# Performance work log

Measured on AMD Instinct MI355X. Metric: run time of the kernel, lower is better.

The kernel has to match this reference:

```python
import jax, jax.numpy as jnp
import numpy as np
from jax import lax

EPS = 1e-5
TEM = 10.0  # self.tem at init; tem_proportion buffer is 0 so it stays 10.0


def _conv1d(x, w, padding, dilation=1, groups=1):
    # x: [B, C, S], w: [O, I//groups, K]
    return lax.conv_general_dilated(
        x, w, window_strides=(1,), padding=[(padding, padding)],
        rhs_dilation=(dilation,), dimension_numbers=('NCH', 'OIH', 'NCH'),
        feature_group_count=groups)


def _bn(y, gamma, beta):
    # training-mode BatchNorm1d: stats over (batch, length) per channel
    m = y.mean(axis=(0, 2), keepdims=True)
    v = y.var(axis=(0, 2), keepdims=True)
    return (y - m) * lax.rsqrt(v + EPS) * gamma[None, :, None] + beta[None, :, None]


def _nor_conv(x, w, g, b, k):
    return _bn(_conv1d(jax.nn.relu(x), w, padding=k // 2), g, b)


def _dil_conv(x, wd, wp, g, b, k):
    C = x.shape[1]
    y = _conv1d(jax.nn.relu(x), wd, padding=k - 1, dilation=2, groups=C)
    y = _conv1d(y, wp, padding=0)
    return _bn(y, g, b)


def _avg_pool3(x):
    s = lax.reduce_window(x, 0.0, lax.add, (1, 1, 3), (1, 1, 1),
                          [(0, 0), (0, 0), (1, 1)])
    return s / 3.0  # count_include_pad=True


def _max_pool3(x):
    return lax.reduce_window(x, -jnp.inf, lax.max, (1, 1, 3), (1, 1, 1),
                             [(0, 0), (0, 0), (1, 1)])


def _forward(x, u, arch_parameters,
             w_nor3, g_nor3, b_nor3, w_nor5, g_nor5, b_nor5,
             w_nor7, g_nor7, b_nor7,
             wd_dil3, wp_dil3, g_dil3, b_dil3,
             wd_dil5, wp_dil5, g_dil5, b_dil5,
             wd_dil7, wp_dil7, g_dil7, b_dil7):
    # ---- Gumbel straight-through gate (get_gumbel_prob) ----
    uc = jnp.clip(u, 1e-9, 1.0 - 1e-9)
    gumbels = -jnp.log(-jnp.log(uc))  # -log(Exp(1) sample)
    logits = (jax.nn.log_softmax(arch_parameters, axis=1) + gumbels) / TEM
    probs = jax.nn.softmax(logits, axis=1)          # [1, 10]
    index = jnp.argmax(probs, axis=-1)              # [1]
    one_h = jax.nn.one_hot(index, probs.shape[-1], dtype=probs.dtype)
    hardwts = one_h - lax.stop_gradient(probs) + probs  # straight-through

    # ---- forward_gdas: single edge (max_nodes=2) ----
    xc = jnp.transpose(x, (0, 2, 1))  # [B, H, S]: hidden=channels, seq=length
    branches = [
        lambda t: jnp.zeros_like(t),                         # none
        _avg_pool3,                                          # avg_pool_3
        _max_pool3,                                          # max_pool_3
        lambda t: _nor_conv(t, w_nor3, g_nor3, b_nor3, 3),   # nor_conv_3
        lambda t: _nor_conv(t, w_nor5, g_nor5, b_nor5, 5),   # nor_conv_5
        lambda t: _nor_conv(t, w_nor7, g_nor7, b_nor7, 7),   # nor_conv_7
        lambda t: _dil_conv(t, wd_dil3, wp_dil3, g_dil3, b_dil3, 3),
        lambda t: _dil_conv(t, wd_dil5, wp_dil5, g_dil5, b_dil5, 5),
        lambda t: _dil_conv(t, wd_dil7, wp_dil7, g_dil7, b_dil7, 7),
        lambda t: t,                                         # skip_connect
    ]
    idx = index[0]
    w = hardwts[0]                                  # [10]
    sel = lax.switch(idx, branches, xc)             # only argmax op is run
    w_sel = jnp.take(w, idx)
    # GDAS: w[argmax]*op(x) + sum of remaining scalar weights (broadcast add)
    out = w_sel * sel + (jnp.sum(w) - w_sel)
    out = jnp.transpose(out, (0, 2, 1))             # back to [B, S, H]
    return out + x                                  # residual


def setup_inputs() -> dict:
    key = jax.random.key(0)
    ks = jax.random.split(key, 16)
    B, S, H = 8, 512, 768
    d = {
        'x': jax.random.normal(ks[0], (B, S, H), jnp.float32),
        'u': jax.random.uniform(ks[1], (1, 10), jnp.float32),
        'arch_parameters': 0.001 * jax.random.normal(ks[2], (1, 10), jnp.float32),
    }
    i = 3
    for k in (3, 5, 7):
        d[f'w_nor{k}'] = 0.02 * jax.random.normal(ks[i], (H, H, k), jnp.float32); i += 1
        d[f'g_nor{k}'] = jnp.ones((H,), jnp.float32)
        d[f'b_nor{k}'] = jnp.zeros((H,), jnp.float32)
    for k in (3, 5, 7):
        d[f'wd_dil{k}'] = 0.1 * jax.random.normal(ks[i], (H, 1, k), jnp.float32); i += 1
        d[f'wp_dil{k}'] = 0.02 * jax.random.normal(ks[i], (H, H, 1), jnp.float32); i += 1
        d[f'g_dil{k}'] = jnp.ones((H,), jnp.float32)
        d[f'b_dil{k}'] = jnp.zeros((H,), jnp.float32)
    return d


def reference(x, u, arch_parameters,
              w_nor3, g_nor3, b_nor3, w_nor5, g_nor5, b_nor5,
              w_nor7, g_nor7, b_nor7,
              wd_dil3, wp_dil3, g_dil3, b_dil3,
              wd_dil5, wp_dil5, g_dil5, b_dil5,
              wd_dil7, wp_dil7, g_dil7, b_dil7):
    return _forward(x, u, arch_parameters,
                    w_nor3, g_nor3, b_nor3, w_nor5, g_nor5, b_nor5,
                    w_nor7, g_nor7, b_nor7,
                    wd_dil3, wp_dil3, g_dil3, b_dil3,
                    wd_dil5, wp_dil5, g_dil5, b_dil5,
                    wd_dil7, wp_dil7, g_dil7, b_dil7)
```

## Files before the change

kernel.cpp:

```cpp
#include <hip/hip_runtime.h>
#include <math.h>

#define BB 8
#define SS 512
#define HH 768
#define NTOT (BB*SS*HH)
#define EPSBN 1e-5f
#define SPAD 4
#define SROWS (SS + 2*SPAD)

typedef __attribute__((ext_vector_type(8))) short short8v;
typedef __attribute__((ext_vector_type(4))) float float4v;

struct Params {
  const float *x, *u, *ap;
  const float *w_nor3, *g_nor3, *b_nor3;
  const float *w_nor5, *g_nor5, *b_nor5;
  const float *w_nor7, *g_nor7, *b_nor7;
  const float *wd3, *wp3, *gd3, *bd3;
  const float *wd5, *wp5, *gd5, *bd5;
  const float *wd7, *wp7, *gd7, *bd7;
  float *out;
  float *hdr;
  float *y;
  short *xb;
  short *wb;
  float *psum;
  float *psq;
};

__device__ __forceinline__ short f2bf(float f) {
  union { float f; unsigned u; } v; v.f = f;
  unsigned r = v.u + 0x7FFF + ((v.u >> 16) & 1);
  return (short)(r >> 16);
}

__global__ void gate_kernel(Params p) {
  int t = threadIdx.x;
  for (int i = t; i < HH; i += 64) { p.psum[i] = 0.f; p.psq[i] = 0.f; }
  if (t != 0) return;
  float ap[10], lg[10], pr[10];
  float mx = -INFINITY;
  for (int i = 0; i < 10; i++) { ap[i] = p.ap[i]; mx = fmaxf(mx, ap[i]); }
  float se = 0.f;
  for (int i = 0; i < 10; i++) se += expf(ap[i] - mx);
  float lse = mx + logf(se);
  float lmax = -INFINITY;
  for (int i = 0; i < 10; i++) {
    float uc = fminf(fmaxf(p.u[i], 1e-9f), 1.f - 1e-9f);
    float gb = -logf(-logf(uc));
    lg[i] = ((ap[i] - lse) + gb) * 0.1f;
    lmax = fmaxf(lmax, lg[i]);
  }
  float ps = 0.f;
  for (int i = 0; i < 10; i++) { pr[i] = expf(lg[i] - lmax); ps += pr[i]; }
  int idx = 0; float best = -INFINITY;
  for (int i = 0; i < 10; i++) {
    pr[i] /= ps;
    if (pr[i] > best) { best = pr[i]; idx = i; }
  }
  float w_sel = (1.0f - pr[idx]) + pr[idx];
  p.hdr[0] = w_sel;
  p.hdr[1] = 0.0f;
  ((int*)p.hdr)[2] = idx;
}

#define XBLK 1560
#define WBLK 2016
__global__ __launch_bounds__(256) void prep_kernel(Params p) {
  int idx = ((const int*)p.hdr)[2];
  if (idx < 3 || idx > 8) return;
  int t = threadIdx.x;
  if (blockIdx.x < XBLK) {
    int u = blockIdx.x * 256 + t;
    int c0 = (u % 96) * 8;
    int row = (u / 96) % SROWS;
    int b = u / (96 * SROWS);
    int s = row - SPAD;
    short8v o8 = (short8v){0,0,0,0,0,0,0,0};
    if (s >= 0 && s < SS) {
      float v[8];
      if (idx <= 5) {
        const float* xp = p.x + ((size_t)(b * SS + s) * HH + c0);
        float4 f0 = ((const float4*)xp)[0];
        float4 f1 = ((const float4*)xp)[1];
        v[0] = fmaxf(f0.x, 0.f); v[1] = fmaxf(f0.y, 0.f);
        v[2] = fmaxf(f0.z, 0.f); v[3] = fmaxf(f0.w, 0.f);
        v[4] = fmaxf(f1.x, 0.f); v[5] = fmaxf(f1.y, 0.f);
        v[6] = fmaxf(f1.z, 0.f); v[7] = fmaxf(f1.w, 0.f);
      } else {
        int k = 3 + 2 * (idx - 6);
        const float* wd = (idx == 6) ? p.wd3 : (idx == 7) ? p.wd5 : p.wd7;
#pragma unroll
        for (int j = 0; j < 8; j++) v[j] = 0.f;
        for (int dk = 0; dk < k; dk++) {
          int ss = s + 2 * dk - (k - 1);
          if (ss < 0 || ss >= SS) continue;
          const float* xp = p.x + ((size_t)(b * SS + ss) * HH + c0);
          float4 f0 = ((const float4*)xp)[0];
          float4 f1 = ((const float4*)xp)[1];
          float ff[8] = {f0.x, f0.y, f0.z, f0.w, f1.x, f1.y, f1.z, f1.w};
#pragma unroll
          for (int j = 0; j < 8; j++)
            v[j] += fmaxf(ff[j], 0.f) * wd[(c0 + j) * k + dk];
        }
      }
#pragma unroll
      for (int j = 0; j < 8; j++) o8[j] = f2bf(v[j]);
    }
    *(short8v*)(p.xb + (size_t)(b * SROWS + row) * HH + c0) = o8;
  } else {
    int u = (blockIdx.x - XBLK) * 256 + t;
    int i0 = (u % 96) * 8;
    int o = (u / 96) % HH;
    int dk = u / (96 * HH);
    short8v o8;
    if (idx <= 5) {
      int k = 3 + 2 * (idx - 3);
      if (dk >= k) return;
      const float* W = (idx == 3) ? p.w_nor3 : (idx == 4) ? p.w_nor5 : p.w_nor7;
#pragma unroll
      for (int j = 0; j < 8; j++)
        o8[j] = f2bf(W[((size_t)o * HH + i0 + j) * k + dk]);
      *(short8v*)(p.wb + ((size_t)dk * HH + o) * HH + i0) = o8;
    } else {
      if (dk != 0) return;
      const float* W = (idx == 6) ? p.wp3 : (idx == 7) ? p.wp5 : p.wp7;
      const float* wp0 = W + (size_t)o * HH + i0;
      float4 f0 = ((const float4*)wp0)[0];
      float4 f1 = ((const float4*)wp0)[1];
      o8[0] = f2bf(f0.x); o8[1] = f2bf(f0.y); o8[2] = f2bf(f0.z); o8[3] = f2bf(f0.w);
      o8[4] = f2bf(f1.x); o8[5] = f2bf(f1.y); o8[6] = f2bf(f1.z); o8[7] = f2bf(f1.w);
      *(short8v*)(p.wb + (size_t)o * HH + i0) = o8;
    }
  }
}

#define BM 128
#define BN 64
#define BK 64

typedef const __attribute__((address_space(1))) unsigned int* gas_t;
typedef __attribute__((address_space(3))) unsigned int* las_t;
__device__ __forceinline__ void gload16(const void* g, void* l) {
  __builtin_amdgcn_global_load_lds((gas_t)g, (las_t)l, 16, 0, 0);
}

__global__ __launch_bounds__(256) void conv_gemm_kernel(Params p) {
  int idx = ((const int*)p.hdr)[2];
  if (idx < 3 || idx > 8) return;
  bool nor = (idx <= 5);
  int taps = nor ? (3 + 2 * (idx - 3)) : 1;
  int halo = nor ? (taps >> 1) : 0;

  __shared__ __attribute__((aligned(16))) short As[BM * BK];
  __shared__ __attribute__((aligned(16))) short Bs[BN * BK];

  int mt = blockIdx.x;
  int b = mt >> 2;
  int s0 = (mt & 3) * BM;
  int o0 = blockIdx.y * BN;

  int t = threadIdx.x;
  int lane = t & 63;
  int w = t >> 6;
  int l16 = lane & 15, quad = lane >> 4;
  int wm0 = (w >> 1) * 64;
  int wn0 = (w & 1) * 32;
  int lr = lane >> 3;
  int sw8 = ((lane & 7) ^ lr) * 8;

  short* Al0 = &As[(32 * w) * BK];
  short* Bl0 = &Bs[(16 * w) * BK];

  float4v acc[4][2];
#pragma unroll
  for (int mi = 0; mi < 4; mi++)
#pragma unroll
    for (int ni = 0; ni < 2; ni++) acc[mi][ni] = (float4v){0.f, 0.f, 0.f, 0.f};

  const char* Ac = (const char*)As;
  const char* Bc = (const char*)Bs;
  int aro[4], bro[2], co[2];
#pragma unroll
  for (int mi = 0; mi < 4; mi++) aro[mi] = (wm0 + mi * 16 + l16) * (BK * 2);
#pragma unroll
  for (int ni = 0; ni < 2; ni++) bro[ni] = (wn0 + ni * 16 + l16) * (BK * 2);
  int sx = (l16 & 7) << 4;
  co[0] = (quad * 16) ^ sx;
  co[1] = (64 + quad * 16) ^ sx;

  for (int dk = 0; dk < taps; dk++) {
    int shift = dk - halo;
    const short* Ag[4]; const short* Bg[2];
#pragma unroll
    for (int j = 0; j < 4; j++) {
      int tr = 32 * w + 8 * j + lr;
      Ag[j] = p.xb + (size_t)(b * SROWS + SPAD + s0 + shift + tr) * HH + sw8;
    }
#pragma unroll
    for (int j = 0; j < 2; j++) {
      int tr = 16 * w + 8 * j + lr;
      Bg[j] = p.wb + ((size_t)dk * HH + o0 + tr) * HH + sw8;
    }
    for (int k0 = 0; k0 < HH; k0 += BK) {
#pragma unroll
      for (int j = 0; j < 4; j++) gload16(Ag[j] + k0, Al0 + j * 8 * BK);
#pragma unroll
      for (int j = 0; j < 2; j++) gload16(Bg[j] + k0, Bl0 + j * 8 * BK);
      __syncthreads();

      short8v af[4][2], bf[2][2];
#pragma unroll
      for (int mi = 0; mi < 4; mi++) {
        af[mi][0] = *(const short8v*)(Ac + aro[mi] + co[0]);
        af[mi][1] = *(const short8v*)(Ac + aro[mi] + co[1]);
      }
#pragma unroll
      for (int ni = 0; ni < 2; ni++) {
        bf[ni][0] = *(const short8v*)(Bc + bro[ni] + co[0]);
        bf[ni][1] = *(const short8v*)(Bc + bro[ni] + co[1]);
      }
#pragma unroll
      for (int h = 0; h < 2; h++)
#pragma unroll
        for (int mi = 0; mi < 4; mi++)
#pragma unroll
          for (int ni = 0; ni < 2; ni++)
            acc[mi][ni] = __builtin_amdgcn_mfma_f32_16x16x32_bf16(af[mi][h], bf[ni][h], acc[mi][ni], 0, 0, 0);
      __syncthreads();
    }
  }

#pragma unroll
  for (int mi = 0; mi < 4; mi++)
#pragma unroll
    for (int ni = 0; ni < 2; ni++) {
      int col = o0 + wn0 + ni * 16 + l16;
#pragma unroll
      for (int r = 0; r < 4; r++) {
        int row = s0 + wm0 + mi * 16 + quad * 4 + r;
        p.y[((size_t)(b * SS + row)) * HH + col] = acc[mi][ni][r];
      }
    }

#pragma unroll
  for (int ni = 0; ni < 2; ni++) {
    float s = 0.f, q = 0.f;
#pragma unroll
    for (int mi = 0; mi < 4; mi++)
#pragma unroll
      for (int r = 0; r < 4; r++) { float v = acc[mi][ni][r]; s += v; q += v * v; }
    s += __shfl_xor(s, 16); s += __shfl_xor(s, 32);
    q += __shfl_xor(q, 16); q += __shfl_xor(q, 32);
    if (lane < 16) {
      int col = o0 + wn0 + ni * 16 + l16;
      atomicAdd(&p.psum[col], s);
      atomicAdd(&p.psq[col], q);
    }
  }
}

__global__ __launch_bounds__(256) void epilogue_kernel(Params p) {
  int idx = ((const int*)p.hdr)[2];
  float w_sel = p.hdr[0], w_rest = p.hdr[1];
  int t4 = blockIdx.x * 256 + threadIdx.x;
  int base = t4 * 4;
  float4 xv = *(const float4*)(p.x + base);
  float4 sel;
  if (idx >= 3 && idx <= 8) {
    const float* g = (idx == 3) ? p.g_nor3 : (idx == 4) ? p.g_nor5 : (idx == 5) ? p.g_nor7
                   : (idx == 6) ? p.gd3 : (idx == 7) ? p.gd5 : p.gd7;
    const float* be = (idx == 3) ? p.b_nor3 : (idx == 4) ? p.b_nor5 : (idx == 5) ? p.b_nor7
                    : (idx == 6) ? p.bd3 : (idx == 7) ? p.bd5 : p.bd7;
    int c = base % HH;
    float4 yv = *(const float4*)(p.y + base);
    float4 ps = *(const float4*)(p.psum + c);
    float4 pq = *(const float4*)(p.psq + c);
    float4 gv = *(const float4*)(g + c);
    float4 bv = *(const float4*)(be + c);
    const float inv = 1.f / 4096.f;
    float m0 = ps.x * inv, m1 = ps.y * inv, m2 = ps.z * inv, m3 = ps.w * inv;
    float i0 = rsqrtf(pq.x * inv - m0 * m0 + EPSBN);
    float i1 = rsqrtf(pq.y * inv - m1 * m1 + EPSBN);
    float i2 = rsqrtf(pq.z * inv - m2 * m2 + EPSBN);
    float i3 = rsqrtf(pq.w * inv - m3 * m3 + EPSBN);
    sel.x = (yv.x - m0) * i0 * gv.x + bv.x;
    sel.y = (yv.y - m1) * i1 * gv.y + bv.y;
    sel.z = (yv.z - m2) * i2 * gv.z + bv.z;
    sel.w = (yv.w - m3) * i3 * gv.w + bv.w;
  } else if (idx == 0) {
    sel = (float4){0.f, 0.f, 0.f, 0.f};
  } else if (idx == 9) {
    sel = xv;
  } else {
    int s = (base / HH) % SS;
    float4 xm, xp;
    if (idx == 1) {
      xm = (s > 0)      ? *(const float4*)(p.x + base - HH) : (float4){0.f, 0.f, 0.f, 0.f};
      xp = (s < SS - 1) ? *(const float4*)(p.x + base + HH) : (float4){0.f, 0.f, 0.f, 0.f};
      const float th = 1.f / 3.f;
      sel.x = (xm.x + xv.x + xp.x) * th;
      sel.y = (xm.y + xv.y + xp.y) * th;
      sel.z = (xm.z + xv.z + xp.z) * th;
      sel.w = (xm.w + xv.w + xp.w) * th;
    } else {
      xm = (s > 0)      ? *(const float4*)(p.x + base - HH) : (float4){-INFINITY, -INFINITY, -INFINITY, -INFINITY};
      xp = (s < SS - 1) ? *(const float4*)(p.x + base + HH) : (float4){-INFINITY, -INFINITY, -INFINITY, -INFINITY};
      sel.x = fmaxf(fmaxf(xm.x, xv.x), xp.x);
      sel.y = fmaxf(fmaxf(xm.y, xv.y), xp.y);
      sel.z = fmaxf(fmaxf(xm.z, xv.z), xp.z);
      sel.w = fmaxf(fmaxf(xm.w, xv.w), xp.w);
    }
  }
  float4 ov;
  ov.x = w_sel * sel.x + w_rest + xv.x;
  ov.y = w_sel * sel.y + w_rest + xv.y;
  ov.z = w_sel * sel.z + w_rest + xv.z;
  ov.w = w_sel * sel.w + w_rest + xv.w;
  *(float4*)(p.out + base) = ov;
}

extern "C" void kernel_launch(void* const* d_in, const int* in_sizes, int n_in,
                              void* d_out, int out_size, void* d_ws, size_t ws_size,
                              hipStream_t stream) {
  Params p;
  p.x = (const float*)d_in[0];
  p.u = (const float*)d_in[1];
  p.ap = (const float*)d_in[2];
  p.w_nor3 = (const float*)d_in[3];  p.g_nor3 = (const float*)d_in[4];  p.b_nor3 = (const float*)d_in[5];
  p.w_nor5 = (const float*)d_in[6];  p.g_nor5 = (const float*)d_in[7];  p.b_nor5 = (const float*)d_in[8];
  p.w_nor7 = (const float*)d_in[9];  p.g_nor7 = (const float*)d_in[10]; p.b_nor7 = (const float*)d_in[11];
  p.wd3 = (const float*)d_in[12]; p.wp3 = (const float*)d_in[13]; p.gd3 = (const float*)d_in[14]; p.bd3 = (const float*)d_in[15];
  p.wd5 = (const float*)d_in[16]; p.wp5 = (const float*)d_in[17]; p.gd5 = (const float*)d_in[18]; p.bd5 = (const float*)d_in[19];
  p.wd7 = (const float*)d_in[20]; p.wp7 = (const float*)d_in[21]; p.gd7 = (const float*)d_in[22]; p.bd7 = (const float*)d_in[23];
  p.out = (float*)d_out;

  char* ws = (char*)d_ws;
  size_t off = 0;
  p.hdr = (float*)(ws + off); off += 256;
  p.y   = (float*)(ws + off); off += (size_t)NTOT * 4;
  p.xb  = (short*)(ws + off); off += (size_t)BB * SROWS * HH * 2;
  p.wb  = (short*)(ws + off); off += (size_t)7 * HH * HH * 2;
  p.psum = (float*)(ws + off); off += HH * 4;
  p.psq  = (float*)(ws + off); off += HH * 4;

  hipLaunchKernelGGL(gate_kernel, dim3(1), dim3(64), 0, stream, p);
  hipLaunchKernelGGL(prep_kernel, dim3(XBLK + WBLK), dim3(256), 0, stream, p);
  hipLaunchKernelGGL(conv_gemm_kernel, dim3(SS * BB / BM, HH / BN), dim3(256), 0, stream, p);
  hipLaunchKernelGGL(epilogue_kernel, dim3(NTOT / 4 / 256), dim3(256), 0, stream, p);
}
```

Baseline: 137.0 us.

## Reuse halo-extended activation tile across conv taps and vectorize weight prep

```diff
diff --git a/kernel.cpp b/kernel.cpp
--- a/kernel.cpp
+++ b/kernel.cpp
@@ -66,7 +66,24 @@
 }
 
 #define XBLK 1560
-#define WBLK 2016
+#define WBLK 288
+
+template<int K>
+__device__ __forceinline__ void wprep(const float* __restrict__ W, short* __restrict__ wb,
+                                      int o, int i0) {
+  const float* src = W + ((size_t)o * HH + i0) * K;
+  float f[8 * K];
+#pragma unroll
+  for (int j = 0; j < 2 * K; j++) ((float4*)f)[j] = ((const float4*)src)[j];
+#pragma unroll
+  for (int dk = 0; dk < K; dk++) {
+    short8v o8;
+#pragma unroll
+    for (int j = 0; j < 8; j++) o8[j] = f2bf(f[j * K + dk]);
+    *(short8v*)(wb + ((size_t)dk * HH + o) * HH + i0) = o8;
+  }
+}
+
 __global__ __launch_bounds__(256) void prep_kernel(Params p) {
   int idx = ((const int*)p.hdr)[2];
   if (idx < 3 || idx > 8) return;
@@ -112,33 +129,18 @@
   } else {
     int u = (blockIdx.x - XBLK) * 256 + t;
     int i0 = (u % 96) * 8;
-    int o = (u / 96) % HH;
-    int dk = u / (96 * HH);
-    short8v o8;
-    if (idx <= 5) {
-      int k = 3 + 2 * (idx - 3);
-      if (dk >= k) return;
-      const float* W = (idx == 3) ? p.w_nor3 : (idx == 4) ? p.w_nor5 : p.w_nor7;
-#pragma unroll
-      for (int j = 0; j < 8; j++)
-        o8[j] = f2bf(W[((size_t)o * HH + i0 + j) * k + dk]);
-      *(short8v*)(p.wb + ((size_t)dk * HH + o) * HH + i0) = o8;
-    } else {
-      if (dk != 0) return;
-      const float* W = (idx == 6) ? p.wp3 : (idx == 7) ? p.wp5 : p.wp7;
-      const float* wp0 = W + (size_t)o * HH + i0;
-      float4 f0 = ((const float4*)wp0)[0];
-      float4 f1 = ((const float4*)wp0)[1];
-      o8[0] = f2bf(f0.x); o8[1] = f2bf(f0.y); o8[2] = f2bf(f0.z); o8[3] = f2bf(f0.w);
-      o8[4] = f2bf(f1.x); o8[5] = f2bf(f1.y); o8[6] = f2bf(f1.z); o8[7] = f2bf(f1.w);
-      *(short8v*)(p.wb + (size_t)o * HH + i0) = o8;
-    }
+    int o = u / 96;
+    if (idx == 3)      wprep<3>(p.w_nor3, p.wb, o, i0);
+    else if (idx == 4) wprep<5>(p.w_nor5, p.wb, o, i0);
+    else if (idx == 5) wprep<7>(p.w_nor7, p.wb, o, i0);
+    else wprep<1>((idx == 6) ? p.wp3 : (idx == 7) ? p.wp5 : p.wp7, p.wb, o, i0);
   }
 }
 
 #define BM 128
 #define BN 64
 #define BK 64
+#define AROWS 136
 
 typedef const __attribute__((address_space(1))) unsigned int* gas_t;
 typedef __attribute__((address_space(3))) unsigned int* las_t;
@@ -146,15 +148,15 @@
   __builtin_amdgcn_global_load_lds((gas_t)g, (las_t)l, 16, 0, 0);
 }
 
-__global__ __launch_bounds__(256) void conv_gemm_kernel(Params p) {
+__global__ __launch_bounds__(256, 3) void conv_gemm_kernel(Params p) {
   int idx = ((const int*)p.hdr)[2];
   if (idx < 3 || idx > 8) return;
   bool nor = (idx <= 5);
   int taps = nor ? (3 + 2 * (idx - 3)) : 1;
   int halo = nor ? (taps >> 1) : 0;
 
-  __shared__ __attribute__((aligned(16))) short As[BM * BK];
-  __shared__ __attribute__((aligned(16))) short Bs[BN * BK];
+  __shared__ __attribute__((aligned(16))) short As[AROWS * BK];
+  __shared__ __attribute__((aligned(16))) short Bs[4 * BN * BK];
 
   int mt = blockIdx.x;
   int b = mt >> 2;
@@ -170,8 +172,18 @@
   int lr = lane >> 3;
   int sw8 = ((lane & 7) ^ lr) * 8;
 
-  short* Al0 = &As[(32 * w) * BK];
-  short* Bl0 = &Bs[(16 * w) * BK];
+  const short* Ag[4];
+  int abrow = b * SROWS + s0 + 8 * w + lr;
+#pragma unroll
+  for (int j = 0; j < 4; j++)
+    Ag[j] = p.xb + (size_t)(abrow + 32 * j) * HH + sw8;
+  const short* Agp = p.xb + (size_t)(b * SROWS + s0 + 128 + lr) * HH + sw8;
+  const short* Bg = p.wb + (size_t)(o0 + 8 * w + lr) * HH + sw8;
+
+  short* Asl[4];
+#pragma unroll
+  for (int j = 0; j < 4; j++) Asl[j] = &As[(32 * j + 8 * w) * BK];
+  short* Aslp = &As[128 * BK];
 
   float4v acc[4][2];
 #pragma unroll
@@ -181,53 +193,66 @@
 
   const char* Ac = (const char*)As;
   const char* Bc = (const char*)Bs;
-  int aro[4], bro[2], co[2];
-#pragma unroll
-  for (int mi = 0; mi < 4; mi++) aro[mi] = (wm0 + mi * 16 + l16) * (BK * 2);
-#pragma unroll
-  for (int ni = 0; ni < 2; ni++) bro[ni] = (wn0 + ni * 16 + l16) * (BK * 2);
-  int sx = (l16 & 7) << 4;
-  co[0] = (quad * 16) ^ sx;
-  co[1] = (64 + quad * 16) ^ sx;
-
-  for (int dk = 0; dk < taps; dk++) {
-    int shift = dk - halo;
-    const short* Ag[4]; const short* Bg[2];
-#pragma unroll
-    for (int j = 0; j < 4; j++) {
-      int tr = 32 * w + 8 * j + lr;
-      Ag[j] = p.xb + (size_t)(b * SROWS + SPAD + s0 + shift + tr) * HH + sw8;
-    }
-#pragma unroll
-    for (int j = 0; j < 2; j++) {
-      int tr = 16 * w + 8 * j + lr;
-      Bg[j] = p.wb + ((size_t)dk * HH + o0 + tr) * HH + sw8;
-    }
-    for (int k0 = 0; k0 < HH; k0 += BK) {
-#pragma unroll
-      for (int j = 0; j < 4; j++) gload16(Ag[j] + k0, Al0 + j * 8 * BK);
-#pragma unroll
-      for (int j = 0; j < 2; j++) gload16(Bg[j] + k0, Bl0 + j * 8 * BK);
+  int bb[2][2];
+#pragma unroll
+  for (int ni = 0; ni < 2; ni++)
+#pragma unroll
+    for (int h = 0; h < 2; h++)
+      bb[ni][h] = (wn0 + ni * 16 + l16) * (2 * BK) + (((h * 4 + quad) ^ (l16 & 7)) << 4);
+
+  int np0 = taps < 4 ? taps : 4;
+  int np1 = taps - np0;
+
+  auto mm = [&](int dk, int pl) {
+    int doff = dk - halo + 4;
+    int rowA = wm0 + l16 + doff;
+    int xr = (l16 + doff) & 7;
+    int a0 = rowA * 128 + ((quad ^ xr) << 4);
+    int a1 = rowA * 128 + (((4 + quad) ^ xr) << 4);
+    short8v af0[4], af1[4], bf0[2], bf1[2];
+#pragma unroll
+    for (int mi = 0; mi < 4; mi++) {
+      af0[mi] = *(const short8v*)(Ac + a0 + mi * 2048);
+      af1[mi] = *(const short8v*)(Ac + a1 + mi * 2048);
+    }
+    int pb = pl * 8192;
+#pragma unroll
+    for (int ni = 0; ni < 2; ni++) {
+      bf0[ni] = *(const short8v*)(Bc + pb + bb[ni][0]);
+      bf1[ni] = *(const short8v*)(Bc + pb + bb[ni][1]);
+    }
+#pragma unroll
+    for (int mi = 0; mi < 4; mi++)
+#pragma unroll
+      for (int ni = 0; ni < 2; ni++)
+        acc[mi][ni] = __builtin_amdgcn_mfma_f32_16x16x32_bf16(af0[mi], bf0[ni], acc[mi][ni], 0, 0, 0);
+#pragma unroll
+    for (int mi = 0; mi < 4; mi++)
+#pragma unroll
+      for (int ni = 0; ni < 2; ni++)
+        acc[mi][ni] = __builtin_amdgcn_mfma_f32_16x16x32_bf16(af1[mi], bf1[ni], acc[mi][ni], 0, 0, 0);
+  };
+
+  for (int k0 = 0; k0 < HH; k0 += BK) {
+#pragma unroll
+    for (int j = 0; j < 4; j++) gload16(Ag[j] + k0, Asl[j]);
+    if (w == 0) gload16(Agp + k0, Aslp);
+    for (int pl = 0; pl < np0; pl++) {
+      const short* src = Bg + (size_t)pl * HH * HH + k0;
+      gload16(src, &Bs[pl * 4096 + w * 512]);
+      gload16(src + (size_t)32 * HH, &Bs[pl * 4096 + 2048 + w * 512]);
+    }
+    __syncthreads();
+    for (int dk = 0; dk < np0; dk++) mm(dk, dk);
+    __syncthreads();
+    if (np1 > 0) {
+      for (int pl = 0; pl < np1; pl++) {
+        const short* src = Bg + (size_t)(4 + pl) * HH * HH + k0;
+        gload16(src, &Bs[pl * 4096 + w * 512]);
+        gload16(src + (size_t)32 * HH, &Bs[pl * 4096 + 2048 + w * 512]);
+      }
       __syncthreads();
-
-      short8v af[4][2], bf[2][2];
-#pragma unroll
-      for (int mi = 0; mi < 4; mi++) {
-        af[mi][0] = *(const short8v*)(Ac + aro[mi] + co[0]);
-        af[mi][1] = *(const short8v*)(Ac + aro[mi] + co[1]);
-      }
-#pragma unroll
-      for (int ni = 0; ni < 2; ni++) {
-        bf[ni][0] = *(const short8v*)(Bc + bro[ni] + co[0]);
-        bf[ni][1] = *(const short8v*)(Bc + bro[ni] + co[1]);
-      }
-#pragma unroll
-      for (int h = 0; h < 2; h++)
-#pragma unroll
-        for (int mi = 0; mi < 4; mi++)
-#pragma unroll
-          for (int ni = 0; ni < 2; ni++)
-            acc[mi][ni] = __builtin_amdgcn_mfma_f32_16x16x32_bf16(af[mi][h], bf[ni][h], acc[mi][ni], 0, 0, 0);
+      for (int dk = 0; dk < np1; dk++) mm(4 + dk, dk);
       __syncthreads();
     }
   }
```

After: 137.1 us. About the same (+0.1%).
